# Performance work log

Hardware: AMD Instinct MI355X
Metric: run time of the kernel (lower is better)

Reference implementation:

```python
import jax, jax.numpy as jnp
import numpy as np

B, T, N, D = 4, 4, 256, 128  # batch, time_steps, num_nodes, features (in==out)
EPS = 1e-5
NEG = -1e9


def _glorot(key, shape):
    fan_in, fan_out = shape[0], shape[1]
    s = float(np.sqrt(6.0 / (fan_in + fan_out)))
    return jax.random.uniform(key, shape, jnp.float32, -s, s)


def setup_inputs() -> dict:
    key = jax.random.key(0)
    ks = jax.random.split(key, 8)
    x = jax.random.normal(ks[0], (B, T, N, D), jnp.float32)
    adj = (jax.random.uniform(ks[1], (N, N)) < 0.05).astype(jnp.float32)
    adj = jnp.maximum(adj, jnp.eye(N, dtype=jnp.float32))
    weight = _glorot(ks[2], (D, D))            # GCN weight [in, out]
    bias = jnp.zeros((D,), jnp.float32)
    att_w1 = _glorot(ks[3], (2 * D, D))        # Linear(2D -> D), column layout
    att_b1 = jnp.zeros((D,), jnp.float32)
    att_w2 = _glorot(ks[4], (D, 1))            # Linear(D -> 1)
    att_b2 = jnp.zeros((1,), jnp.float32)
    ln_gamma = jnp.ones((D,), jnp.float32)
    ln_beta = jnp.zeros((D,), jnp.float32)
    return dict(x=x, adj_matrix=adj, weight=weight, bias=bias,
                att_w1=att_w1, att_b1=att_b1, att_w2=att_w2, att_b2=att_b2,
                ln_gamma=ln_gamma, ln_beta=ln_beta)


def _layer_norm(y, gamma, beta):
    mu = jnp.mean(y, axis=-1, keepdims=True)
    var = jnp.mean(jnp.square(y - mu), axis=-1, keepdims=True)
    return (y - mu) * jax.lax.rsqrt(var + EPS) * gamma + beta


def reference(x, adj_matrix, weight, bias, att_w1, att_b1, att_w2, att_b2,
              ln_gamma, ln_beta):
    d_out = weight.shape[1]
    # split the first attention Linear so cat([h_i, h_j]) @ W1 == h_i@W1a + h_j@W1b
    W1a, W1b = att_w1[:d_out], att_w1[d_out:]
    w2 = att_w2[:, 0]
    mask = adj_matrix[None] == 0  # [1, N, N]

    def step(carry, x_t):  # x_t: [B, N, D]
        h = x_t @ weight + bias                                  # [B, N, D]
        a = h @ W1a                                              # [B, N, D]
        b = h @ W1b                                              # [B, N, D]
        # big intermediate the kernel would fuse away: [B, N, N, D]
        e = jax.nn.leaky_relu(a[:, :, None, :] + b[:, None, :, :] + att_b1, 0.2)
        scores = jnp.einsum('bijd,d->bij', e, w2) + att_b2[0]    # [B, N, N]
        scores = jnp.where(mask, NEG, scores)
        attn = jax.nn.softmax(scores, axis=-1)  # dropout is identity in eval
        agg = jnp.einsum('bij,bjd->bid', attn, h)                # [B, N, D]
        out = _layer_norm(agg + x_t, ln_gamma, ln_beta)          # in==out residual
        return carry, out

    _, ys = jax.lax.scan(step, None, jnp.swapaxes(x, 0, 1))      # [T, B, N, D]
    return jax.nn.relu(jnp.swapaxes(ys, 0, 1))                   # [B, T, N, D]
```

## Files before the change

kernel.cpp:

```cpp
#include <hip/hip_runtime.h>
#include <hip/hip_bf16.h>

#define BT 16
#define NN 256
#define DD 128
#define MROWS (BT*NN)

typedef __bf16 bf16x8 __attribute__((ext_vector_type(8)));
typedef __bf16 bf16x2 __attribute__((ext_vector_type(2)));
typedef float  f32x4  __attribute__((ext_vector_type(4)));

#define LREL(z) ((z) >= 0.0f ? (z) : 0.2f * (z))
#define HS_STRIDE 136

__global__ __launch_bounds__(256) void gemm2_kernel(
        const float* __restrict__ x, const float* __restrict__ weight,
        const float* __restrict__ bias, const float* __restrict__ attw1,
        const float* __restrict__ attb1, const float* __restrict__ adj,
        __bf16* __restrict__ hbuf, __bf16* __restrict__ abuf,
        __bf16* __restrict__ bbuf, int* __restrict__ nbr,
        int* __restrict__ nbr_cnt) {
    int tid = threadIdx.x;
    int w = tid >> 6, l = tid & 63;
    int chunk = blockIdx.x >> 1, parity = blockIdx.x & 1;
    int row0 = chunk * 16;
    int lrow = l & 15, lk8 = (l >> 4) * 8;

    __shared__ __align__(16) __bf16 hs[16][HS_STRIDE];

    if (parity == 0 && w == 0) {
        int i = chunk;
        int cnt = 0;
        const float* adjrow = adj + (size_t)i * NN;
        for (int jt = 0; jt < NN / 64; ++jt) {
            int j = jt * 64 + l;
            float v = adjrow[j];
            unsigned long long mask = __ballot(v != 0.f);
            if (v != 0.f) {
                int pos = cnt + __popcll(mask & ((1ull << l) - 1ull));
                if (pos < 64) nbr[i * 64 + pos] = j;
            }
            cnt += __popcll(mask);
        }
        if (l == 0) nbr_cnt[i] = min(cnt, 64);
    }

    const float* abase = x + (size_t)(row0 + lrow) * DD + lk8;
    bf16x8 af[4];
#pragma unroll
    for (int kt = 0; kt < 4; ++kt) {
        float4 u0 = *(const float4*)(abase + 32 * kt);
        float4 u1 = *(const float4*)(abase + 32 * kt + 4);
        af[kt][0]=(__bf16)u0.x; af[kt][1]=(__bf16)u0.y;
        af[kt][2]=(__bf16)u0.z; af[kt][3]=(__bf16)u0.w;
        af[kt][4]=(__bf16)u1.x; af[kt][5]=(__bf16)u1.y;
        af[kt][6]=(__bf16)u1.z; af[kt][7]=(__bf16)u1.w;
    }

#pragma unroll
    for (int s = 0; s < 2; ++s) {
        int n0 = (w + 4 * s) * 16;
        int ncol = n0 + lrow;
        bf16x8 wf[4];
#pragma unroll
        for (int kt = 0; kt < 4; ++kt) {
            const float* wp = weight + (size_t)(lk8 + 32 * kt) * DD + ncol;
#pragma unroll
            for (int j = 0; j < 8; ++j)
                wf[kt][j] = (__bf16)wp[(size_t)j * DD];
        }
        f32x4 acc = {0.f, 0.f, 0.f, 0.f};
        acc = __builtin_amdgcn_mfma_f32_16x16x32_bf16(af[0], wf[0], acc, 0, 0, 0);
        acc = __builtin_amdgcn_mfma_f32_16x16x32_bf16(af[1], wf[1], acc, 0, 0, 0);
        acc = __builtin_amdgcn_mfma_f32_16x16x32_bf16(af[2], wf[2], acc, 0, 0, 0);
        acc = __builtin_amdgcn_mfma_f32_16x16x32_bf16(af[3], wf[3], acc, 0, 0, 0);

        float bb = bias[ncol];
        int rloc = (l >> 4) * 4;
        __bf16* hout = hbuf + (size_t)(row0 + rloc) * DD + ncol;
#pragma unroll
        for (int r = 0; r < 4; ++r) {
            __bf16 hv = (__bf16)(acc[r] + bb);
            hs[rloc + r][ncol] = hv;
            if (parity == 0) hout[(size_t)r * DD] = hv;
        }
    }

    bf16x8 w1f[2][4];
#pragma unroll
    for (int s = 0; s < 2; ++s) {
        int ncol = (w + 4 * s) * 16 + lrow;
#pragma unroll
        for (int kt = 0; kt < 4; ++kt) {
            const float* wp = attw1 + (size_t)(parity * DD + lk8 + 32 * kt) * DD + ncol;
#pragma unroll
            for (int j = 0; j < 8; ++j)
                w1f[s][kt][j] = (__bf16)wp[(size_t)j * DD];
        }
    }
    __syncthreads();

    bf16x8 ha[4];
#pragma unroll
    for (int kt = 0; kt < 4; ++kt)
        ha[kt] = *(const bf16x8*)(&hs[lrow][lk8 + 32 * kt]);

#pragma unroll
    for (int s = 0; s < 2; ++s) {
        int n0 = (w + 4 * s) * 16;
        int ncol = n0 + lrow;
        f32x4 acc = {0.f, 0.f, 0.f, 0.f};
        acc = __builtin_amdgcn_mfma_f32_16x16x32_bf16(ha[0], w1f[s][0], acc, 0, 0, 0);
        acc = __builtin_amdgcn_mfma_f32_16x16x32_bf16(ha[1], w1f[s][1], acc, 0, 0, 0);
        acc = __builtin_amdgcn_mfma_f32_16x16x32_bf16(ha[2], w1f[s][2], acc, 0, 0, 0);
        acc = __builtin_amdgcn_mfma_f32_16x16x32_bf16(ha[3], w1f[s][3], acc, 0, 0, 0);

        float bb = parity ? attb1[ncol] : 0.f;
        __bf16* dst = (parity ? bbuf : abuf) + (size_t)(row0 + (l >> 4) * 4) * DD + ncol;
#pragma unroll
        for (int r = 0; r < 4; ++r)
            dst[(size_t)r * DD] = (__bf16)(acc[r] + bb);
    }
}

__global__ __launch_bounds__(256) void attn_kernel(
        const __bf16* __restrict__ hbuf, const __bf16* __restrict__ abuf,
        const __bf16* __restrict__ bbuf, const float* __restrict__ x,
        const int* __restrict__ nbr, const int* __restrict__ nbr_cnt,
        const float* __restrict__ w2, const float* __restrict__ gamma,
        const float* __restrict__ beta, float* __restrict__ out) {
    int tid = threadIdx.x;
    int w = tid >> 6, l = tid & 63;
    int i  = (blockIdx.x & 63) * 4 + w;
    int bt = blockIdx.x >> 6;
    int d2 = 2 * l;

    int cnt = nbr_cnt[i];
    int jreg = nbr[i * 64 + l];

    bf16x2 av = *(const bf16x2*)(abuf + (size_t)(bt * NN + i) * DD + d2);
    float a0 = (float)av[0], a1 = (float)av[1];
    float2 wv = *(const float2*)(w2 + d2);
    float w20 = wv.x, w21 = wv.y;
    const __bf16* bbase = bbuf + (size_t)bt * NN * DD;
    const __bf16* hbase = hbuf + (size_t)bt * NN * DD;

    float m = -3.0e38f, dsum = 0.f, acc0 = 0.f, acc1 = 0.f;
    for (int c = 0; c < cnt; c += 4) {
        int i0 = c, i1 = c + 1, i2 = c + 2, i3 = c + 3;
        bool v1 = i1 < cnt, v2 = i2 < cnt, v3 = i3 < cnt;
        int j0 = __shfl(jreg, i0);
        int j1 = v1 ? __shfl(jreg, i1) : i;
        int j2 = v2 ? __shfl(jreg, i2) : i;
        int j3 = v3 ? __shfl(jreg, i3) : i;
        bf16x2 b0 = *(const bf16x2*)(bbase + (size_t)j0 * DD + d2);
        bf16x2 b1 = *(const bf16x2*)(bbase + (size_t)j1 * DD + d2);
        bf16x2 b2 = *(const bf16x2*)(bbase + (size_t)j2 * DD + d2);
        bf16x2 b3 = *(const bf16x2*)(bbase + (size_t)j3 * DD + d2);
        bf16x2 h0 = *(const bf16x2*)(hbase + (size_t)j0 * DD + d2);
        bf16x2 h1 = *(const bf16x2*)(hbase + (size_t)j1 * DD + d2);
        bf16x2 h2 = *(const bf16x2*)(hbase + (size_t)j2 * DD + d2);
        bf16x2 h3 = *(const bf16x2*)(hbase + (size_t)j3 * DD + d2);

        float p0 = LREL(a0 + (float)b0[0]) * w20 + LREL(a1 + (float)b0[1]) * w21;
        float p1 = LREL(a0 + (float)b1[0]) * w20 + LREL(a1 + (float)b1[1]) * w21;
        float p2 = LREL(a0 + (float)b2[0]) * w20 + LREL(a1 + (float)b2[1]) * w21;
        float p3 = LREL(a0 + (float)b3[0]) * w20 + LREL(a1 + (float)b3[1]) * w21;
#pragma unroll
        for (int off = 32; off; off >>= 1) {
            p0 += __shfl_xor(p0, off);
            p1 += __shfl_xor(p1, off);
            p2 += __shfl_xor(p2, off);
            p3 += __shfl_xor(p3, off);
        }
        float pm0 = p0;
        float pm1 = v1 ? p1 : -3.0e38f;
        float pm2 = v2 ? p2 : -3.0e38f;
        float pm3 = v3 ? p3 : -3.0e38f;
        float m_new = fmaxf(m, fmaxf(fmaxf(pm0, pm1), fmaxf(pm2, pm3)));
        float scale = __expf(m - m_new);
        float e0 = __expf(p0 - m_new);
        float e1 = v1 ? __expf(p1 - m_new) : 0.f;
        float e2 = v2 ? __expf(p2 - m_new) : 0.f;
        float e3 = v3 ? __expf(p3 - m_new) : 0.f;
        dsum = dsum * scale + (e0 + e1) + (e2 + e3);
        acc0 = acc0 * scale + e0 * (float)h0[0] + e1 * (float)h1[0]
                            + e2 * (float)h2[0] + e3 * (float)h3[0];
        acc1 = acc1 * scale + e0 * (float)h0[1] + e1 * (float)h1[1]
                            + e2 * (float)h2[1] + e3 * (float)h3[1];
        m = m_new;
    }
    float inv = 1.f / dsum;

    float2 xv = *(const float2*)(x + (size_t)(bt * NN + i) * DD + d2);
    float y0 = acc0 * inv + xv.x;
    float y1 = acc1 * inv + xv.y;

    float s = y0 + y1;
#pragma unroll
    for (int off = 32; off; off >>= 1) s += __shfl_xor(s, off);
    float mu = s * (1.0f / 128.0f);
    float v0 = y0 - mu, v1 = y1 - mu;
    float vs = v0 * v0 + v1 * v1;
#pragma unroll
    for (int off = 32; off; off >>= 1) vs += __shfl_xor(vs, off);
    float rstd = rsqrtf(vs * (1.0f / 128.0f) + 1e-5f);

    float2 gv = *(const float2*)(gamma + d2);
    float2 bv = *(const float2*)(beta + d2);
    float2 ov;
    ov.x = fmaxf(v0 * rstd * gv.x + bv.x, 0.0f);
    ov.y = fmaxf(v1 * rstd * gv.y + bv.y, 0.0f);
    *(float2*)(out + (size_t)(bt * NN + i) * DD + d2) = ov;
}

extern "C" void kernel_launch(void* const* d_in, const int* in_sizes, int n_in,
                              void* d_out, int out_size, void* d_ws, size_t ws_size,
                              hipStream_t stream) {
    const float* x      = (const float*)d_in[0];
    const float* adj    = (const float*)d_in[1];
    const float* weight = (const float*)d_in[2];
    const float* bias   = (const float*)d_in[3];
    const float* attw1  = (const float*)d_in[4];
    const float* attb1  = (const float*)d_in[5];
    const float* attw2  = (const float*)d_in[6];
    const float* gamma  = (const float*)d_in[8];
    const float* beta   = (const float*)d_in[9];
    float* out = (float*)d_out;

    char* p = (char*)d_ws;
    __bf16* hbuf = (__bf16*)p;        p += (size_t)MROWS * DD * 2;
    __bf16* abuf = (__bf16*)p;        p += (size_t)MROWS * DD * 2;
    __bf16* bbuf = (__bf16*)p;        p += (size_t)MROWS * DD * 2;
    int* nbr     = (int*)p;           p += (size_t)NN * 64 * 4;
    int* nbr_cnt = (int*)p;

    gemm2_kernel<<<MROWS / 16 * 2, 256, 0, stream>>>(x, weight, bias, attw1, attb1,
                                                     adj, hbuf, abuf, bbuf,
                                                     nbr, nbr_cnt);
    attn_kernel<<<NN / 4 * BT, 256, 0, stream>>>(hbuf, abuf, bbuf, x, nbr, nbr_cnt,
                                                 attw2, gamma, beta, out);
}
```

Measured before the change: 24.24 us.

## Fuse projection GEMMs and sparse attention into one LDS-resident kernel per time slice

Merges the two kernels into a single 1024-thread kernel where each block recomputes h and the neighbor-side projection for its entire batch-time slice in LDS, then runs the sparse attention and layernorm for 16 nodes. This removes the second launch and the global bf16 round trip of h/a/b buffers, and builds neighbor lists in LDS per block. In exchange each slice's GEMM work and weight loads are repeated across 16 blocks and LDS usage grows large, limiting occupancy to one block per CU.

New measurement: 48.74 us. +101.1%, slower.

```diff
diff --git a/kernel.cpp b/kernel.cpp
--- a/kernel.cpp
+++ b/kernel.cpp
@@ -4,163 +4,160 @@
 #define BT 16
 #define NN 256
 #define DD 128
-#define MROWS (BT*NN)
 
 typedef __bf16 bf16x8 __attribute__((ext_vector_type(8)));
 typedef __bf16 bf16x2 __attribute__((ext_vector_type(2)));
 typedef float  f32x4  __attribute__((ext_vector_type(4)));
 
 #define LREL(z) ((z) >= 0.0f ? (z) : 0.2f * (z))
-#define HS_STRIDE 136
-
-__global__ __launch_bounds__(256) void gemm2_kernel(
-        const float* __restrict__ x, const float* __restrict__ weight,
-        const float* __restrict__ bias, const float* __restrict__ attw1,
-        const float* __restrict__ attb1, const float* __restrict__ adj,
-        __bf16* __restrict__ hbuf, __bf16* __restrict__ abuf,
-        __bf16* __restrict__ bbuf, int* __restrict__ nbr,
-        int* __restrict__ nbr_cnt) {
+#define HSP 136
+#define LDS_BYTES (256*HSP*2 + 256*DD*2 + 16*HSP*2 + 16*64*4)
+
+__global__ __launch_bounds__(1024, 1) void fused_kernel(
+        const float* __restrict__ x, const float* __restrict__ adj,
+        const float* __restrict__ weight, const float* __restrict__ bias,
+        const float* __restrict__ attw1, const float* __restrict__ attb1,
+        const float* __restrict__ w2, const float* __restrict__ gamma,
+        const float* __restrict__ beta, float* __restrict__ out) {
+    extern __shared__ char smem[];
+    __bf16* hs   = (__bf16*)smem;
+    __bf16* bs   = hs + 256 * HSP;
+    __bf16* as_  = bs + 256 * DD;
+    int*    nbrl = (int*)(as_ + 16 * HSP);
+
     int tid = threadIdx.x;
     int w = tid >> 6, l = tid & 63;
-    int chunk = blockIdx.x >> 1, parity = blockIdx.x & 1;
-    int row0 = chunk * 16;
+    int bt = blockIdx.x >> 4, grp = blockIdx.x & 15;
     int lrow = l & 15, lk8 = (l >> 4) * 8;
-
-    __shared__ __align__(16) __bf16 hs[16][HS_STRIDE];
-
-    if (parity == 0 && w == 0) {
-        int i = chunk;
-        int cnt = 0;
-        const float* adjrow = adj + (size_t)i * NN;
+    int rsub = (l >> 4) * 4;
+
+    int i_node = grp * 16 + w;
+    int cnt = 0;
+    {
+        const float* adjrow = adj + (size_t)i_node * NN;
         for (int jt = 0; jt < NN / 64; ++jt) {
             int j = jt * 64 + l;
             float v = adjrow[j];
             unsigned long long mask = __ballot(v != 0.f);
             if (v != 0.f) {
                 int pos = cnt + __popcll(mask & ((1ull << l) - 1ull));
-                if (pos < 64) nbr[i * 64 + pos] = j;
+                if (pos < 64) nbrl[w * 64 + pos] = j;
             }
             cnt += __popcll(mask);
         }
-        if (l == 0) nbr_cnt[i] = min(cnt, 64);
-    }
-
-    const float* abase = x + (size_t)(row0 + lrow) * DD + lk8;
-    bf16x8 af[4];
+        cnt = min(cnt, 64);
+    }
+
+    int ct = w & 7, half = w >> 3;
+    int ncol = ct * 16 + lrow;
+
+    bf16x8 wf[4], w1bf[4];
 #pragma unroll
     for (int kt = 0; kt < 4; ++kt) {
-        float4 u0 = *(const float4*)(abase + 32 * kt);
-        float4 u1 = *(const float4*)(abase + 32 * kt + 4);
-        af[kt][0]=(__bf16)u0.x; af[kt][1]=(__bf16)u0.y;
-        af[kt][2]=(__bf16)u0.z; af[kt][3]=(__bf16)u0.w;
-        af[kt][4]=(__bf16)u1.x; af[kt][5]=(__bf16)u1.y;
-        af[kt][6]=(__bf16)u1.z; af[kt][7]=(__bf16)u1.w;
-    }
-
-#pragma unroll
-    for (int s = 0; s < 2; ++s) {
-        int n0 = (w + 4 * s) * 16;
-        int ncol = n0 + lrow;
-        bf16x8 wf[4];
+        const float* wp = weight + (size_t)(lk8 + 32 * kt) * DD + ncol;
+        const float* bp = attw1 + (size_t)(DD + lk8 + 32 * kt) * DD + ncol;
+#pragma unroll
+        for (int j = 0; j < 8; ++j) {
+            wf[kt][j]   = (__bf16)wp[(size_t)j * DD];
+            w1bf[kt][j] = (__bf16)bp[(size_t)j * DD];
+        }
+    }
+    bf16x8 w1af[4];
+    if (w < 8) {
 #pragma unroll
         for (int kt = 0; kt < 4; ++kt) {
-            const float* wp = weight + (size_t)(lk8 + 32 * kt) * DD + ncol;
+            const float* ap = attw1 + (size_t)(lk8 + 32 * kt) * DD + (w * 16 + lrow);
 #pragma unroll
             for (int j = 0; j < 8; ++j)
-                wf[kt][j] = (__bf16)wp[(size_t)j * DD];
+                w1af[kt][j] = (__bf16)ap[(size_t)j * DD];
+        }
+    }
+
+    float bb = bias[ncol];
+#pragma unroll
+    for (int rt8 = 0; rt8 < 8; ++rt8) {
+        int rt = half * 8 + rt8;
+        const float* abase = x + ((size_t)bt * NN + rt * 16 + lrow) * DD + lk8;
+        bf16x8 af[4];
+#pragma unroll
+        for (int kt = 0; kt < 4; ++kt) {
+            float4 u0 = *(const float4*)(abase + 32 * kt);
+            float4 u1 = *(const float4*)(abase + 32 * kt + 4);
+            af[kt][0]=(__bf16)u0.x; af[kt][1]=(__bf16)u0.y;
+            af[kt][2]=(__bf16)u0.z; af[kt][3]=(__bf16)u0.w;
+            af[kt][4]=(__bf16)u1.x; af[kt][5]=(__bf16)u1.y;
+            af[kt][6]=(__bf16)u1.z; af[kt][7]=(__bf16)u1.w;
         }
         f32x4 acc = {0.f, 0.f, 0.f, 0.f};
         acc = __builtin_amdgcn_mfma_f32_16x16x32_bf16(af[0], wf[0], acc, 0, 0, 0);
         acc = __builtin_amdgcn_mfma_f32_16x16x32_bf16(af[1], wf[1], acc, 0, 0, 0);
         acc = __builtin_amdgcn_mfma_f32_16x16x32_bf16(af[2], wf[2], acc, 0, 0, 0);
         acc = __builtin_amdgcn_mfma_f32_16x16x32_bf16(af[3], wf[3], acc, 0, 0, 0);
-
-        float bb = bias[ncol];
-        int rloc = (l >> 4) * 4;
-        __bf16* hout = hbuf + (size_t)(row0 + rloc) * DD + ncol;
-#pragma unroll
-        for (int r = 0; r < 4; ++r) {
-            __bf16 hv = (__bf16)(acc[r] + bb);
-            hs[rloc + r][ncol] = hv;
-            if (parity == 0) hout[(size_t)r * DD] = hv;
-        }
-    }
-
-    bf16x8 w1f[2][4];
-#pragma unroll
-    for (int s = 0; s < 2; ++s) {
-        int ncol = (w + 4 * s) * 16 + lrow;
-#pragma unroll
-        for (int kt = 0; kt < 4; ++kt) {
-            const float* wp = attw1 + (size_t)(parity * DD + lk8 + 32 * kt) * DD + ncol;
-#pragma unroll
-            for (int j = 0; j < 8; ++j)
-                w1f[s][kt][j] = (__bf16)wp[(size_t)j * DD];
-        }
+        int row0 = rt * 16 + rsub;
+#pragma unroll
+        for (int r = 0; r < 4; ++r)
+            hs[(size_t)(row0 + r) * HSP + ncol] = (__bf16)(acc[r] + bb);
     }
     __syncthreads();
 
-    bf16x8 ha[4];
-#pragma unroll
-    for (int kt = 0; kt < 4; ++kt)
-        ha[kt] = *(const bf16x8*)(&hs[lrow][lk8 + 32 * kt]);
-
-#pragma unroll
-    for (int s = 0; s < 2; ++s) {
-        int n0 = (w + 4 * s) * 16;
-        int ncol = n0 + lrow;
+    float bb1 = attb1[ncol];
+#pragma unroll
+    for (int rt8 = 0; rt8 < 8; ++rt8) {
+        int rt = half * 8 + rt8;
+        bf16x8 ha[4];
+#pragma unroll
+        for (int kt = 0; kt < 4; ++kt)
+            ha[kt] = *(const bf16x8*)&hs[(size_t)(rt * 16 + lrow) * HSP + lk8 + 32 * kt];
         f32x4 acc = {0.f, 0.f, 0.f, 0.f};
-        acc = __builtin_amdgcn_mfma_f32_16x16x32_bf16(ha[0], w1f[s][0], acc, 0, 0, 0);
-        acc = __builtin_amdgcn_mfma_f32_16x16x32_bf16(ha[1], w1f[s][1], acc, 0, 0, 0);
-        acc = __builtin_amdgcn_mfma_f32_16x16x32_bf16(ha[2], w1f[s][2], acc, 0, 0, 0);
-        acc = __builtin_amdgcn_mfma_f32_16x16x32_bf16(ha[3], w1f[s][3], acc, 0, 0, 0);
-
-        float bb = parity ? attb1[ncol] : 0.f;
-        __bf16* dst = (parity ? bbuf : abuf) + (size_t)(row0 + (l >> 4) * 4) * DD + ncol;
+        acc = __builtin_amdgcn_mfma_f32_16x16x32_bf16(ha[0], w1bf[0], acc, 0, 0, 0);
+        acc = __builtin_amdgcn_mfma_f32_16x16x32_bf16(ha[1], w1bf[1], acc, 0, 0, 0);
+        acc = __builtin_amdgcn_mfma_f32_16x16x32_bf16(ha[2], w1bf[2], acc, 0, 0, 0);
+        acc = __builtin_amdgcn_mfma_f32_16x16x32_bf16(ha[3], w1bf[3], acc, 0, 0, 0);
+        int row0 = rt * 16 + rsub;
 #pragma unroll
         for (int r = 0; r < 4; ++r)
-            dst[(size_t)r * DD] = (__bf16)(acc[r] + bb);
-    }
-}
-
-__global__ __launch_bounds__(256) void attn_kernel(
-        const __bf16* __restrict__ hbuf, const __bf16* __restrict__ abuf,
-        const __bf16* __restrict__ bbuf, const float* __restrict__ x,
-        const int* __restrict__ nbr, const int* __restrict__ nbr_cnt,
-        const float* __restrict__ w2, const float* __restrict__ gamma,
-        const float* __restrict__ beta, float* __restrict__ out) {
-    int tid = threadIdx.x;
-    int w = tid >> 6, l = tid & 63;
-    int i  = (blockIdx.x & 63) * 4 + w;
-    int bt = blockIdx.x >> 6;
+            bs[(size_t)(row0 + r) * DD + ncol] = (__bf16)(acc[r] + bb1);
+    }
+
+    if (w < 8) {
+        int ncol2 = w * 16 + lrow;
+        bf16x8 hg[4];
+#pragma unroll
+        for (int kt = 0; kt < 4; ++kt)
+            hg[kt] = *(const bf16x8*)&hs[(size_t)(grp * 16 + lrow) * HSP + lk8 + 32 * kt];
+        f32x4 acc = {0.f, 0.f, 0.f, 0.f};
+        acc = __builtin_amdgcn_mfma_f32_16x16x32_bf16(hg[0], w1af[0], acc, 0, 0, 0);
+        acc = __builtin_amdgcn_mfma_f32_16x16x32_bf16(hg[1], w1af[1], acc, 0, 0, 0);
+        acc = __builtin_amdgcn_mfma_f32_16x16x32_bf16(hg[2], w1af[2], acc, 0, 0, 0);
+        acc = __builtin_amdgcn_mfma_f32_16x16x32_bf16(hg[3], w1af[3], acc, 0, 0, 0);
+#pragma unroll
+        for (int r = 0; r < 4; ++r)
+            as_[(size_t)(rsub + r) * HSP + ncol2] = (__bf16)acc[r];
+    }
+    __syncthreads();
+
     int d2 = 2 * l;
-
-    int cnt = nbr_cnt[i];
-    int jreg = nbr[i * 64 + l];
-
-    bf16x2 av = *(const bf16x2*)(abuf + (size_t)(bt * NN + i) * DD + d2);
+    int jreg = nbrl[w * 64 + l];
+    bf16x2 av = *(const bf16x2*)(as_ + (size_t)w * HSP + d2);
     float a0 = (float)av[0], a1 = (float)av[1];
     float2 wv = *(const float2*)(w2 + d2);
     float w20 = wv.x, w21 = wv.y;
-    const __bf16* bbase = bbuf + (size_t)bt * NN * DD;
-    const __bf16* hbase = hbuf + (size_t)bt * NN * DD;
 
     float m = -3.0e38f, dsum = 0.f, acc0 = 0.f, acc1 = 0.f;
     for (int c = 0; c < cnt; c += 4) {
-        int i0 = c, i1 = c + 1, i2 = c + 2, i3 = c + 3;
-        bool v1 = i1 < cnt, v2 = i2 < cnt, v3 = i3 < cnt;
-        int j0 = __shfl(jreg, i0);
-        int j1 = v1 ? __shfl(jreg, i1) : i;
-        int j2 = v2 ? __shfl(jreg, i2) : i;
-        int j3 = v3 ? __shfl(jreg, i3) : i;
-        bf16x2 b0 = *(const bf16x2*)(bbase + (size_t)j0 * DD + d2);
-        bf16x2 b1 = *(const bf16x2*)(bbase + (size_t)j1 * DD + d2);
-        bf16x2 b2 = *(const bf16x2*)(bbase + (size_t)j2 * DD + d2);
-        bf16x2 b3 = *(const bf16x2*)(bbase + (size_t)j3 * DD + d2);
-        bf16x2 h0 = *(const bf16x2*)(hbase + (size_t)j0 * DD + d2);
-        bf16x2 h1 = *(const bf16x2*)(hbase + (size_t)j1 * DD + d2);
-        bf16x2 h2 = *(const bf16x2*)(hbase + (size_t)j2 * DD + d2);
-        bf16x2 h3 = *(const bf16x2*)(hbase + (size_t)j3 * DD + d2);
+        bool v1 = c + 1 < cnt, v2 = c + 2 < cnt, v3 = c + 3 < cnt;
+        int j0 = __shfl(jreg, c);
+        int j1 = v1 ? __shfl(jreg, c + 1) : i_node;
+        int j2 = v2 ? __shfl(jreg, c + 2) : i_node;
+        int j3 = v3 ? __shfl(jreg, c + 3) : i_node;
+        bf16x2 b0 = *(const bf16x2*)(bs + (size_t)j0 * DD + d2);
+        bf16x2 b1 = *(const bf16x2*)(bs + (size_t)j1 * DD + d2);
+        bf16x2 b2 = *(const bf16x2*)(bs + (size_t)j2 * DD + d2);
+        bf16x2 b3 = *(const bf16x2*)(bs + (size_t)j3 * DD + d2);
+        bf16x2 h0 = *(const bf16x2*)(hs + (size_t)j0 * HSP + d2);
+        bf16x2 h1 = *(const bf16x2*)(hs + (size_t)j1 * HSP + d2);
+        bf16x2 h2 = *(const bf16x2*)(hs + (size_t)j2 * HSP + d2);
+        bf16x2 h3 = *(const bf16x2*)(hs + (size_t)j3 * HSP + d2);
 
         float p0 = LREL(a0 + (float)b0[0]) * w20 + LREL(a1 + (float)b0[1]) * w21;
         float p1 = LREL(a0 + (float)b1[0]) * w20 + LREL(a1 + (float)b1[1]) * w21;
@@ -173,11 +170,10 @@
             p2 += __shfl_xor(p2, off);
             p3 += __shfl_xor(p3, off);
         }
-        float pm0 = p0;
         float pm1 = v1 ? p1 : -3.0e38f;
         float pm2 = v2 ? p2 : -3.0e38f;
         float pm3 = v3 ? p3 : -3.0e38f;
-        float m_new = fmaxf(m, fmaxf(fmaxf(pm0, pm1), fmaxf(pm2, pm3)));
+        float m_new = fmaxf(m, fmaxf(fmaxf(p0, pm1), fmaxf(pm2, pm3)));
         float scale = __expf(m - m_new);
         float e0 = __expf(p0 - m_new);
         float e1 = v1 ? __expf(p1 - m_new) : 0.f;
@@ -192,7 +188,7 @@
     }
     float inv = 1.f / dsum;
 
-    float2 xv = *(const float2*)(x + (size_t)(bt * NN + i) * DD + d2);
+    float2 xv = *(const float2*)(x + ((size_t)bt * NN + i_node) * DD + d2);
     float y0 = acc0 * inv + xv.x;
     float y1 = acc1 * inv + xv.y;
 
@@ -211,7 +207,7 @@
     float2 ov;
     ov.x = fmaxf(v0 * rstd * gv.x + bv.x, 0.0f);
     ov.y = fmaxf(v1 * rstd * gv.y + bv.y, 0.0f);
-    *(float2*)(out + (size_t)(bt * NN + i) * DD + d2) = ov;
+    *(float2*)(out + ((size_t)bt * NN + i_node) * DD + d2) = ov;
 }
 
 extern "C" void kernel_launch(void* const* d_in, const int* in_sizes, int n_in,
@@ -228,16 +224,6 @@
     const float* beta   = (const float*)d_in[9];
     float* out = (float*)d_out;
 
-    char* p = (char*)d_ws;
-    __bf16* hbuf = (__bf16*)p;        p += (size_t)MROWS * DD * 2;
-    __bf16* abuf = (__bf16*)p;        p += (size_t)MROWS * DD * 2;
-    __bf16* bbuf = (__bf16*)p;        p += (size_t)MROWS * DD * 2;
-    int* nbr     = (int*)p;           p += (size_t)NN * 64 * 4;
-    int* nbr_cnt = (int*)p;
-
-    gemm2_kernel<<<MROWS / 16 * 2, 256, 0, stream>>>(x, weight, bias, attw1, attb1,
-                                                     adj, hbuf, abuf, bbuf,
-                                                     nbr, nbr_cnt);
-    attn_kernel<<<NN / 4 * BT, 256, 0, stream>>>(hbuf, abuf, bbuf, x, nbr, nbr_cnt,
-                                                 attw2, gamma, beta, out);
+    fused_kernel<<<BT * 16, 1024, LDS_BYTES, stream>>>(
+        x, adj, weight, bias, attw1, attb1, attw2, gamma, beta, out);
 }
```
